# Kernel tuning notes

Hardware: AMD Instinct MI355X
Metric: run time of the kernel (lower is better)

Reference implementation:

```python
import jax, jax.numpy as jnp
import numpy as np

EPS = 1e-5  # torch BatchNorm2d default


def _conv(x, w, padding):
    return jax.lax.conv_general_dilated(
        x, w, window_strides=(1, 1),
        padding=[(padding, padding), (padding, padding)],
        dimension_numbers=("NCHW", "OIHW", "NCHW"))


def _bn(x, gamma, beta):
    # training-mode batchnorm (biased variance), matching nn.BatchNorm2d forward
    mu = x.mean(axis=(0, 2, 3), keepdims=True)
    var = x.var(axis=(0, 2, 3), keepdims=True)
    xn = (x - mu) * jax.lax.rsqrt(var + EPS)
    return gamma[None, :, None, None] * xn + beta[None, :, None, None]


def _ste(x):
    # forward: sign(x); backward: pass gradient where |x| <= 1 (STE)
    m = (jnp.abs(x) <= 1.0).astype(x.dtype)
    s = jax.lax.stop_gradient(jnp.sign(x))
    return s + m * x - jax.lax.stop_gradient(m * x)


def _binconv(x, w, alpha, padding=1):
    # XNOR-style: sign both operands, full-precision conv, scale by alpha
    return _conv(jnp.sign(x), jnp.sign(w), padding) * alpha


def _maxpool2(x):
    return jax.lax.reduce_window(x, -jnp.inf, jax.lax.max,
                                 (1, 1, 2, 2), (1, 1, 2, 2), "VALID")


def setup_inputs() -> dict:
    key = jax.random.key(0)
    ks = jax.random.split(key, 8)

    def kaiming(k, shape):
        fan_out = shape[0] * shape[2] * shape[3]
        std = np.sqrt(2.0 / fan_out)
        return jax.random.normal(k, shape, dtype=jnp.float32) * std

    return {
        "x": jax.random.normal(ks[0], (128, 1, 128, 128), dtype=jnp.float32),
        # first conv (full precision) 1->32, k=3, pad=1
        "w1": kaiming(ks[1], (32, 1, 3, 3)),
        "b1": jnp.zeros((32,), jnp.float32),
        "g1": jnp.ones((32,), jnp.float32),
        "beta1": jnp.zeros((32,), jnp.float32),
        # BinaryConv2d 32->32
        "w2": kaiming(ks[2], (32, 32, 3, 3)),
        "a2": jnp.ones((1,), jnp.float32),
        "g2": jnp.ones((32,), jnp.float32),
        "beta2": jnp.zeros((32,), jnp.float32),
        # BinaryConv2d 32->64
        "w3": kaiming(ks[3], (64, 32, 3, 3)),
        "a3": jnp.ones((1,), jnp.float32),
        "g3": jnp.ones((64,), jnp.float32),
        "beta3": jnp.zeros((64,), jnp.float32),
        # BinaryConv2d 64->128
        "w4": kaiming(ks[4], (128, 64, 3, 3)),
        "a4": jnp.ones((1,), jnp.float32),
        # classifier 128->10
        "wf": jax.random.normal(ks[5], (10, 128), dtype=jnp.float32) * (1.0 / np.sqrt(128.0)),
        "bf": jnp.zeros((10,), jnp.float32),
    }


def reference(x, w1, b1, g1, beta1, w2, a2, g2, beta2, w3, a3, g3, beta3, w4, a4, wf, bf):
    h = _conv(x, w1, padding=1) + b1[None, :, None, None]   # [N,32,128,128]
    h = _bn(h, g1, beta1)
    h = _ste(h)
    h = _binconv(h, w2, a2)                                 # [N,32,128,128]
    h = _maxpool2(h)                                        # [N,32,64,64]
    h = _bn(h, g2, beta2)
    h = _ste(h)
    h = _binconv(h, w3, a3)                                 # [N,64,64,64]
    h = _maxpool2(h)                                        # [N,64,32,32]
    h = _bn(h, g3, beta3)
    h = _ste(h)
    h = _binconv(h, w4, a4)                                 # [N,128,32,32]
    h = h.mean(axis=(2, 3))                                 # AdaptiveAvgPool2d(1) -> [N,128]
    return h @ wf.T + bf                                    # [N,10]
```

## Files before the change

### kernel.cpp

```cpp
#include <hip/hip_runtime.h>
#include <stdint.h>

constexpr int NB = 128;

__global__ void pack_weights_all_kernel(const float* __restrict__ w2, const float* __restrict__ w3,
                                        const float* __restrict__ w4,
                                        uint32_t* __restrict__ wp2, uint32_t* __restrict__ wp3,
                                        uint32_t* __restrict__ wp4)
{
    int idx = blockIdx.x * blockDim.x + threadIdx.x;
    const float* w; uint32_t* o; int ICW, i;
    if (idx < 288)       { w = w2; o = wp2; ICW = 1; i = idx; }
    else if (idx < 864)  { w = w3; o = wp3; ICW = 1; i = idx - 288; }
    else if (idx < 3168) { w = w4; o = wp4; ICW = 2; i = idx - 864; }
    else return;
    int iw = i % ICW;
    int t  = (i / ICW) % 9;
    int oc = i / (9 * ICW);
    int IC = ICW * 32;
    uint32_t word = 0;
    for (int b = 0; b < 32; ++b) {
        float wv = w[(size_t)(oc * IC + (iw * 32 + b)) * 9 + t];
        word |= (wv > 0.f ? 1u : 0u) << b;
    }
    o[i] = word;
}

__global__ void zero_borders_kernel(uint32_t* __restrict__ s1p, uint32_t* __restrict__ s2p,
                                    uint32_t* __restrict__ counters)
{
    int t = blockIdx.x * 256 + threadIdx.x;
    if (t < 4) counters[t] = 0u;
    const int total1 = 128 * 516;
    if (t < total1) {
        int n = t / 516, i = t % 516;
        int r, c;
        if (i < 130)      { r = 0;   c = i; }
        else if (i < 260) { r = 129; c = i - 130; }
        else { int j = i - 260; r = 1 + (j >> 1); c = (j & 1) ? 129 : 0; }
        s1p[(size_t)n * 16900 + r * 130 + c] = 0u;
    }
    int t2 = t - total1;
    const int total2 = 128 * 260;
    if (t2 >= 0 && t2 < total2) {
        int n = t2 / 260, i = t2 % 260;
        int r, c;
        if (i < 66)       { r = 0;  c = i; }
        else if (i < 132) { r = 65; c = i - 66; }
        else { int j = i - 132; r = 1 + (j >> 1); c = (j & 1) ? 65 : 0; }
        s2p[(size_t)n * 4356 + r * 66 + c] = 0u;
    }
}

__device__ __forceinline__ void conv1_load9(const float* __restrict__ x, int p, float* xv)
{
    int n = p >> 14;
    int y = (p >> 7) & 127;
    int c = p & 127;
    const float* xn = x + (size_t)n * 16384;
    #pragma unroll
    for (int ky = 0; ky < 3; ++ky)
    #pragma unroll
    for (int kx = 0; kx < 3; ++kx) {
        int yy = y + ky - 1, cc = c + kx - 1;
        float v = 0.f;
        if (yy >= 0 && yy < 128 && cc >= 0 && cc < 128) v = xn[yy * 128 + cc];
        xv[ky * 3 + kx] = v;
    }
}

__global__ __launch_bounds__(256) void xcorr_kernel(const float* __restrict__ x,
                                                    float* __restrict__ partials)
{
    __shared__ float wbuf[4][64];
    int tid = threadIdx.x;
    float s[9], c[45];
    #pragma unroll
    for (int t = 0; t < 9; ++t) s[t] = 0.f;
    #pragma unroll
    for (int q = 0; q < 45; ++q) c[q] = 0.f;

    int base = blockIdx.x * 256 + tid;
    #pragma unroll 4
    for (int k = 0; k < 16; ++k) {
        float xv[9];
        conv1_load9(x, base + k * 131072, xv);
        #pragma unroll
        for (int t = 0; t < 9; ++t) {
            s[t] += xv[t];
            #pragma unroll
            for (int u = t; u < 9; ++u) {
                int q = t * (19 - t) / 2 + (u - t);
                c[q] = fmaf(xv[t], xv[u], c[q]);
            }
        }
    }
    #pragma unroll
    for (int t = 0; t < 9; ++t) {
        float a = s[t];
        #pragma unroll
        for (int off = 32; off >= 1; off >>= 1) a += __shfl_xor(a, off, 64);
        s[t] = a;
    }
    #pragma unroll
    for (int q = 0; q < 45; ++q) {
        float a = c[q];
        #pragma unroll
        for (int off = 32; off >= 1; off >>= 1) a += __shfl_xor(a, off, 64);
        c[q] = a;
    }
    int lane = tid & 63, wv = tid >> 6;
    if (lane == 0) {
        #pragma unroll
        for (int t = 0; t < 9; ++t) wbuf[wv][t] = s[t];
        #pragma unroll
        for (int q = 0; q < 45; ++q) wbuf[wv][9 + q] = c[q];
    }
    __syncthreads();
    if (tid < 54)
        partials[blockIdx.x * 64 + tid] =
            (wbuf[0][tid] + wbuf[1][tid]) + (wbuf[2][tid] + wbuf[3][tid]);
}

__global__ __launch_bounds__(512) void reduce_ss1_kernel(
    const float* __restrict__ partials, const float* __restrict__ w1, const float* __restrict__ b1,
    const float* __restrict__ g1, const float* __restrict__ be1,
    float* __restrict__ ss, float* __restrict__ w1f)
{
    __shared__ double red[54][8];
    __shared__ double S[9], C[45];
    int tid = threadIdx.x;
    int ch = tid >> 3, part = tid & 7;
    if (ch < 54) {
        double a0 = 0.0, a1 = 0.0, a2 = 0.0, a3 = 0.0;
        #pragma unroll 4
        for (int j = 0; j < 64; ++j) {
            double v = (double)partials[(size_t)(part + 8 * j) * 64 + ch];
            if ((j & 3) == 0) a0 += v;
            else if ((j & 3) == 1) a1 += v;
            else if ((j & 3) == 2) a2 += v;
            else a3 += v;
        }
        red[ch][part] = (a0 + a1) + (a2 + a3);
    }
    __syncthreads();
    if (tid < 54) {
        double a = 0.0;
        #pragma unroll
        for (int i = 0; i < 8; ++i) a += red[tid][i];
        if (tid < 9) S[tid] = a;
        else C[tid - 9] = a;
    }
    __syncthreads();
    if (tid >= 32) return;
    double b = (double)b1[tid];
    double w[9];
    #pragma unroll
    for (int t = 0; t < 9; ++t) w[t] = (double)w1[tid * 9 + t];
    double Sdot = 0.0, Q = 0.0;
    #pragma unroll
    for (int t = 0; t < 9; ++t) {
        Sdot += w[t] * S[t];
        #pragma unroll
        for (int u = t; u < 9; ++u) {
            int q = t * (19 - t) / 2 + (u - t);
            double term = w[t] * w[u] * C[q];
            Q += (u == t) ? term : 2.0 * term;
        }
    }
    const double N = 2097152.0;
    double mu  = Sdot / N + b;
    double ex2 = (Q + 2.0 * b * Sdot) / N + b * b;
    float var = (float)(ex2 - mu * mu);
    float A = g1[tid] * (1.f / sqrtf(var + 1e-5f));
    ss[tid] = A;
    ss[32 + tid] = be1[tid] - (float)mu * A;
    #pragma unroll
    for (int t = 0; t < 9; ++t) w1f[tid * 12 + t] = w1[tid * 9 + t];
    w1f[tid * 12 + 9]  = A;
    w1f[tid * 12 + 10] = fmaf(A, b1[tid], be1[tid] - (float)mu * A);
    w1f[tid * 12 + 11] = 0.f;
}

__global__ __launch_bounds__(256) void conv1_pack4_kernel(
    const float* __restrict__ x, const float* __restrict__ w1f, uint32_t* __restrict__ s1p)
{
    __shared__ float wl[384];
    int tid = threadIdx.x;
    if (tid < 96) ((float4*)wl)[tid] = ((const float4*)w1f)[tid];
    __syncthreads();

    int t = blockIdx.x * 256 + tid;
    int n = t >> 12;
    int y = (t >> 5) & 127;
    int q = t & 31;
    int c0 = q << 2;
    const float* xn = x + (size_t)n * 16384;

    float xv[3][6];
    #pragma unroll
    for (int r = 0; r < 3; ++r) {
        int yy = y - 1 + r;
        bool rv = (yy >= 0) && (yy < 128);
        float4 v = {0.f, 0.f, 0.f, 0.f};
        float lf = 0.f, rt = 0.f;
        if (rv) {
            v = *(const float4*)(xn + yy * 128 + c0);
            if (q != 0)  lf = xn[yy * 128 + c0 - 1];
            if (q != 31) rt = xn[yy * 128 + c0 + 4];
        }
        xv[r][0] = lf; xv[r][1] = v.x; xv[r][2] = v.y;
        xv[r][3] = v.z; xv[r][4] = v.w; xv[r][5] = rt;
    }

    uint32_t word[4] = {0u, 0u, 0u, 0u};
    for (int oc = 0; oc < 32; ++oc) {
        float4 wa = *(const float4*)&wl[oc * 12];
        float4 wb = *(const float4*)&wl[oc * 12 + 4];
        float4 wc = *(const float4*)&wl[oc * 12 + 8];
        float w[9] = {wa.x, wa.y, wa.z, wa.w, wb.x, wb.y, wb.z, wb.w, wc.x};
        #pragma unroll
        for (int i = 0; i < 4; ++i) {
            float a = xv[0][i] * w[0];
            a = fmaf(xv[0][i + 1], w[1], a);
            a = fmaf(xv[0][i + 2], w[2], a);
            a = fmaf(xv[1][i],     w[3], a);
            a = fmaf(xv[1][i + 1], w[4], a);
            a = fmaf(xv[1][i + 2], w[5], a);
            a = fmaf(xv[2][i],     w[6], a);
            a = fmaf(xv[2][i + 1], w[7], a);
            a = fmaf(xv[2][i + 2], w[8], a);
            float vv = fmaf(wc.y, a, wc.z);
            word[i] |= (vv > 0.f ? 1u : 0u) << oc;
        }
    }
    size_t base = (size_t)n * 16900 + (size_t)(y + 1) * 130 + (c0 + 1);
    #pragma unroll
    for (int i = 0; i < 4; ++i) s1p[base + i] = word[i];
}

template<int OC, int PW, int LPW, int MAINB>
__global__ __launch_bounds__(256) void binconv_mainfix_kernel(
    const uint32_t* __restrict__ sp_in, const uint32_t* __restrict__ wp,
    const float* __restrict__ alpha, uint32_t* __restrict__ m16)
{
    constexpr int PS = 2 * PW + 2;
    constexpr int TOTAL = NB * PW * PW;
    __shared__ uint32_t wl[OC * 12];
    int tid = threadIdx.x;
    for (int i = tid; i < OC * 9; i += 256) wl[(i / 9) * 12 + (i % 9)] = wp[i];
    __syncthreads();
    bool useMax = (alpha[0] >= 0.f);

    if ((int)blockIdx.x < MAINB) {
        int p = blockIdx.x * 256 + tid;
        int px = p & (PW - 1), py = (p >> LPW) & (PW - 1), n = p >> (2 * LPW);
        bool border = (px == 0) | (px == PW - 1) | (py == 0) | (py == PW - 1);
        const uint32_t* base = sp_in + (size_t)n * PS * PS + (2 * py) * PS + 2 * px;

        uint32_t xw[16];
        #pragma unroll
        for (int r = 0; r < 4; ++r) {
            uint2 a = *(const uint2*)(base + r * PS);
            uint2 b = *(const uint2*)(base + r * PS + 2);
            xw[r * 4 + 0] = a.x; xw[r * 4 + 1] = a.y;
            xw[r * 4 + 2] = b.x; xw[r * 4 + 3] = b.y;
        }

        uint32_t pend = 0;
        for (int oc = 0; oc < OC; ++oc) {
            uint4 wa = *(const uint4*)&wl[oc * 12];
            uint4 wb = *(const uint4*)&wl[oc * 12 + 4];
            uint32_t w8 = wl[oc * 12 + 8];
            uint32_t w[9] = {wa.x, wa.y, wa.z, wa.w, wb.x, wb.y, wb.z, wb.w, w8};
            int s0 = 0, s1 = 0, s2 = 0, s3 = 0;
            #pragma unroll
            for (int ky = 0; ky < 3; ++ky)
            #pragma unroll
            for (int kx = 0; kx < 3; ++kx) {
                uint32_t wt = w[ky * 3 + kx];
                s0 += __popc(xw[ky * 4 + kx]           ^ wt);
                s1 += __popc(xw[ky * 4 + kx + 1]       ^ wt);
                s2 += __popc(xw[(ky + 1) * 4 + kx]     ^ wt);
                s3 += __popc(xw[(ky + 1) * 4 + kx + 1] ^ wt);
            }
            int sm = useMax ? min(min(s0, s1), min(s2, s3))
                            : max(max(s0, s1), max(s2, s3));
            int m = 288 - 2 * sm;
            if ((oc & 1) == 0) pend = (uint32_t)(uint16_t)(short)m;
            else if (!border)
                m16[(size_t)(oc >> 1) * TOTAL + p] = pend | ((uint32_t)(uint16_t)(short)m << 16);
        }
    } else {
        constexpr int RING = 4 * PW - 4;
        int t = ((int)blockIdx.x - MAINB) * 256 + tid;
        if (t >= NB * RING) return;
        int n = t / RING, r = t % RING;
        int py, px;
        if (r < PW)              { py = 0;      px = r; }
        else if (r < 2 * PW)     { py = PW - 1; px = r - PW; }
        else if (r < 3 * PW - 2) { px = 0;      py = r - 2 * PW + 1; }
        else                     { px = PW - 1; py = r - (3 * PW - 2) + 1; }
        int p = n * PW * PW + py * PW + px;
        const uint32_t* base = sp_in + (size_t)n * PS * PS + (2 * py) * PS + 2 * px;

        uint32_t xw[16], wm[16];
        #pragma unroll
        for (int a = 0; a < 4; ++a) {
            int rr = 2 * py - 1 + a;
            bool rv = (rr >= 0) && (rr < 2 * PW);
            #pragma unroll
            for (int b = 0; b < 4; ++b) {
                int cc = 2 * px - 1 + b;
                bool v = rv && (cc >= 0) && (cc < 2 * PW);
                wm[a * 4 + b] = v ? 0xFFFFFFFFu : 0u;
                xw[a * 4 + b] = base[a * PS + b];
            }
        }
        int cnt[4];
        #pragma unroll
        for (int a2 = 0; a2 < 2; ++a2)
        #pragma unroll
        for (int b2 = 0; b2 < 2; ++b2) {
            int cc = 0;
            #pragma unroll
            for (int ky = 0; ky < 3; ++ky)
            #pragma unroll
            for (int kx = 0; kx < 3; ++kx)
                cc += (int)(wm[(a2 + ky) * 4 + (b2 + kx)] & 1u);
            cnt[a2 * 2 + b2] = cc * 32;
        }

        uint32_t pend = 0;
        for (int oc = 0; oc < OC; ++oc) {
            uint4 wa = *(const uint4*)&wl[oc * 12];
            uint4 wb = *(const uint4*)&wl[oc * 12 + 4];
            uint32_t w8 = wl[oc * 12 + 8];
            uint32_t w[9] = {wa.x, wa.y, wa.z, wa.w, wb.x, wb.y, wb.z, wb.w, w8};
            int v[4];
            #pragma unroll
            for (int a2 = 0; a2 < 2; ++a2)
            #pragma unroll
            for (int b2 = 0; b2 < 2; ++b2) {
                int pop = 0;
                #pragma unroll
                for (int ky = 0; ky < 3; ++ky)
                #pragma unroll
                for (int kx = 0; kx < 3; ++kx) {
                    int idx = (a2 + ky) * 4 + (b2 + kx);
                    pop += __popc((xw[idx] ^ w[ky * 3 + kx]) & wm[idx]);
                }
                v[a2 * 2 + b2] = cnt[a2 * 2 + b2] - 2 * pop;
            }
            int m = useMax ? max(max(v[0], v[1]), max(v[2], v[3]))
                           : min(min(v[0], v[1]), min(v[2], v[3]));
            if ((oc & 1) == 0) pend = (uint32_t)(uint16_t)(short)m;
            else m16[(size_t)(oc >> 1) * TOTAL + p] = pend | ((uint32_t)(uint16_t)(short)m << 16);
        }
    }
}

template<int PIXELS, int CHUNKS, int OC>
__global__ __launch_bounds__(256) void stats16_fin_kernel(
    const uint32_t* __restrict__ m16, double* __restrict__ pd, uint32_t* __restrict__ counter,
    const float* __restrict__ gamma, const float* __restrict__ beta,
    const float* __restrict__ alpha, float inv_n, float* __restrict__ ss)
{
    __shared__ int wb[4][4];
    int bid = blockIdx.x;
    int q = bid / CHUNKS, ch = bid % CHUNKS;
    const uint32_t* pl = m16 + (size_t)q * PIXELS + (size_t)ch * (PIXELS / CHUNKS);
    int tid = threadIdx.x;
    int s0 = 0, s1 = 0, q0 = 0, q1 = 0;
    #pragma unroll 4
    for (int j = 0; j < PIXELS / CHUNKS / 256; ++j) {
        uint32_t u = pl[tid + j * 256];
        int m0 = (int)(short)(u & 0xffffu);
        int m1 = (int)u >> 16;
        s0 += m0; s1 += m1;
        q0 += m0 * m0; q1 += m1 * m1;
    }
    #pragma unroll
    for (int off = 32; off >= 1; off >>= 1) {
        s0 += __shfl_xor(s0, off, 64); s1 += __shfl_xor(s1, off, 64);
        q0 += __shfl_xor(q0, off, 64); q1 += __shfl_xor(q1, off, 64);
    }
    int lane = tid & 63, w = tid >> 6;
    if (lane == 0) { wb[w][0] = s0; wb[w][1] = s1; wb[w][2] = q0; wb[w][3] = q1; }
    __syncthreads();
    if (tid < 4)
        pd[(size_t)bid * 4 + tid] =
            (double)((long long)wb[0][tid] + wb[1][tid] + wb[2][tid] + wb[3][tid]);

    __threadfence();
    __shared__ int lastflag;
    if (tid == 0) lastflag = (atomicAdd(counter, 1u) == (uint32_t)(gridDim.x - 1)) ? 1 : 0;
    __syncthreads();
    if (!lastflag) return;
    __threadfence();
    if (tid == 0) *counter = 0u;

    __shared__ double sums[2 * OC];
    if (tid < 2 * OC) {
        bool issq = tid >= OC;
        int c = issq ? tid - OC : tid;
        int qq = c >> 1;
        int slot = (issq ? 2 : 0) + (c & 1);
        double a = 0.0;
        #pragma unroll 4
        for (int i = 0; i < CHUNKS; ++i)
            a += pd[(size_t)(qq * CHUNKS + i) * 4 + slot];
        sums[tid] = a;
    }
    __syncthreads();
    if (tid < OC) {
        double al = (double)alpha[0];
        float mu  = (float)(sums[tid] * al * (double)inv_n);
        float ex2 = (float)(sums[OC + tid] * al * al * (double)inv_n);
        float var = ex2 - mu * mu;
        float A = gamma[tid] * (1.f / sqrtf(var + 1e-5f));
        ss[tid] = A;
        ss[OC + tid] = beta[tid] - mu * A;
    }
}

template<int OC, int PW, int LPW, bool PADOUT>
__global__ __launch_bounds__(256) void binconv_pack_kernel(
    const uint32_t* __restrict__ m16, const float* __restrict__ alpha,
    const float* __restrict__ ss, void* __restrict__ sout)
{
    constexpr int TOTAL = NB * PW * PW;
    __shared__ float Ap[OC], Bp[OC];
    int tid = threadIdx.x;
    if (tid < OC) { Ap[tid] = ss[tid] * alpha[0]; Bp[tid] = ss[OC + tid]; }
    __syncthreads();
    int p = blockIdx.x * 256 + tid;
    uint64_t word = 0;
    #pragma unroll
    for (int q = 0; q < OC / 2; ++q) {
        uint32_t u = m16[(size_t)q * TOTAL + p];
        int m0 = (int)(short)(u & 0xffffu);
        int m1 = (int)u >> 16;
        float v0 = fmaf(Ap[2 * q],     (float)m0, Bp[2 * q]);
        float v1 = fmaf(Ap[2 * q + 1], (float)m1, Bp[2 * q + 1]);
        word |= (v0 > 0.f ? 1ull : 0ull) << (2 * q);
        word |= (v1 > 0.f ? 1ull : 0ull) << (2 * q + 1);
    }
    if constexpr (PADOUT) {
        int px = p & (PW - 1), py = (p >> LPW) & (PW - 1), n = p >> (2 * LPW);
        ((uint32_t*)sout)[(size_t)n * (PW + 2) * (PW + 2) + (py + 1) * (PW + 2) + (px + 1)]
            = (uint32_t)word;
    } else {
        ((uint64_t*)sout)[p] = word;
    }
}

__global__ __launch_bounds__(256) void conv4_partial_kernel(
    const uint64_t* __restrict__ s3, const uint64_t* __restrict__ wp4,
    float* __restrict__ p4)
{
    __shared__ uint64_t xt[192];
    __shared__ uint64_t wl[1152];
    __shared__ float red[256];
    int b = blockIdx.x;
    int n = b >> 3, s = b & 7;
    int tid = threadIdx.x;
    for (int i = tid; i < 192; i += 256) {
        int row = 4 * s - 1 + (i >> 5);
        int col = i & 31;
        xt[i] = (row >= 0 && row < 32) ? s3[(size_t)n * 1024 + row * 32 + col] : 0ull;
    }
    for (int i = tid; i < 1152; i += 256) wl[i] = wp4[i];
    __syncthreads();
    int oc = tid & 127, h = tid >> 7;
    uint64_t wr[9];
    #pragma unroll
    for (int t = 0; t < 9; ++t) wr[t] = wl[oc * 9 + t];
    int acc = 0;
    #pragma unroll
    for (int ry = 0; ry < 2; ++ry) {
        int lry = 2 * h + ry;
        int y = 4 * s + lry;
        for (int x = 0; x < 32; ++x) {
            int pop = 0, c = 0;
            #pragma unroll
            for (int ky = 0; ky < 3; ++ky) {
                int yy = y + ky - 1;
                if (yy < 0 || yy >= 32) continue;
                int lrow = lry + ky;
                #pragma unroll
                for (int kx = 0; kx < 3; ++kx) {
                    int xx = x + kx - 1;
                    if (xx < 0 || xx >= 32) continue;
                    pop += __popcll(xt[lrow * 32 + xx] ^ wr[ky * 3 + kx]);
                    c += 64;
                }
            }
            acc += c - 2 * pop;
        }
    }
    red[tid] = (float)acc;
    __syncthreads();
    if (tid < 128)
        p4[(size_t)b * 128 + tid] = red[tid] + red[tid + 128];
}

__global__ __launch_bounds__(128) void mean_linear_kernel(
    const float* __restrict__ p4, const float* __restrict__ alpha4,
    const float* __restrict__ wf, const float* __restrict__ bf, float* __restrict__ out)
{
    __shared__ float ml[128];
    int n = blockIdx.x, tid = threadIdx.x;
    float a = 0.f;
    #pragma unroll
    for (int s = 0; s < 8; ++s)
        a += p4[(size_t)((n * 8 + s) * 128) + tid];
    ml[tid] = a * alpha4[0] * (1.f / 1024.f);
    __syncthreads();
    if (tid < 10) {
        const float* w = wf + tid * 128;
        float acc = bf[tid];
        #pragma unroll 4
        for (int i = 0; i < 128; ++i) acc = fmaf(ml[i], w[i], acc);
        out[n * 10 + tid] = acc;
    }
}

extern "C" void kernel_launch(void* const* d_in, const int* in_sizes, int n_in,
                              void* d_out, int out_size, void* d_ws, size_t ws_size,
                              hipStream_t stream)
{
    const float* x   = (const float*)d_in[0];
    const float* w1  = (const float*)d_in[1];
    const float* b1  = (const float*)d_in[2];
    const float* g1  = (const float*)d_in[3];
    const float* be1 = (const float*)d_in[4];
    const float* w2  = (const float*)d_in[5];
    const float* a2  = (const float*)d_in[6];
    const float* g2  = (const float*)d_in[7];
    const float* be2 = (const float*)d_in[8];
    const float* w3  = (const float*)d_in[9];
    const float* a3  = (const float*)d_in[10];
    const float* g3  = (const float*)d_in[11];
    const float* be3 = (const float*)d_in[12];
    const float* w4  = (const float*)d_in[13];
    const float* a4  = (const float*)d_in[14];
    const float* wf  = (const float*)d_in[15];
    const float* bf  = (const float*)d_in[16];
    float* out = (float*)d_out;

    uint8_t* ws = (uint8_t*)d_ws;
    size_t off = 0;
    auto alloc = [&](size_t bytes) -> void* {
        void* p = ws + off;
        off += (bytes + 255) & ~(size_t)255;
        return p;
    };
    uint32_t* wp2 = (uint32_t*)alloc(288 * 4);
    uint32_t* wp3 = (uint32_t*)alloc(576 * 4);
    uint32_t* wp4 = (uint32_t*)alloc(2304 * 4);
    float* ss1 = (float*)alloc(64 * 4);
    float* ss2 = (float*)alloc(64 * 4);
    float* ss3 = (float*)alloc(128 * 4);
    float* w1f = (float*)alloc(384 * 4);
    uint32_t* counters = (uint32_t*)alloc(4 * 4);
    double* pd    = (double*)alloc(2048 * 8);
    float* partials = (float*)alloc((size_t)512 * 64 * 4);
    uint32_t* s1p = (uint32_t*)alloc((size_t)128 * 16900 * 4);
    uint32_t* s2p = (uint32_t*)alloc((size_t)128 * 4356 * 4);
    uint64_t* s3  = (uint64_t*)alloc((size_t)128 * 1024 * 8);
    float* p4    = (float*)alloc((size_t)1024 * 128 * 4);
    uint32_t* m16_2 = (uint32_t*)alloc((size_t)16 * 524288 * 4);
    uint32_t* m16_3 = (uint32_t*)alloc((size_t)32 * 131072 * 4);

    zero_borders_kernel<<<388, 256, 0, stream>>>(s1p, s2p, counters);

    pack_weights_all_kernel<<<13, 256, 0, stream>>>(w2, w3, w4, wp2, wp3, wp4);

    xcorr_kernel<<<512, 256, 0, stream>>>(x, partials);
    reduce_ss1_kernel<<<1, 512, 0, stream>>>(partials, w1, b1, g1, be1, ss1, w1f);
    conv1_pack4_kernel<<<2048, 256, 0, stream>>>(x, w1f, s1p);

    binconv_mainfix_kernel<32, 64, 6, 2048><<<2048 + 126, 256, 0, stream>>>(s1p, wp2, a2, m16_2);
    stats16_fin_kernel<524288, 32, 32><<<512, 256, 0, stream>>>(m16_2, pd, counters + 0,
                                                                g2, be2, a2, 1.f / 524288.f, ss2);
    binconv_pack_kernel<32, 64, 6, true><<<2048, 256, 0, stream>>>(m16_2, a2, ss2, (void*)s2p);

    binconv_mainfix_kernel<64, 32, 5, 512><<<512 + 62, 256, 0, stream>>>(s2p, wp3, a3, m16_3);
    stats16_fin_kernel<131072, 8, 64><<<256, 256, 0, stream>>>(m16_3, pd, counters + 1,
                                                               g3, be3, a3, 1.f / 131072.f, ss3);
    binconv_pack_kernel<64, 32, 5, false><<<512, 256, 0, stream>>>(m16_3, a3, ss3, (void*)s3);

    conv4_partial_kernel<<<1024, 256, 0, stream>>>(s3, (const uint64_t*)wp4, p4);
    mean_linear_kernel<<<128, 128, 0, stream>>>(p4, a4, wf, bf, out);
}
```

Measured before the change: 265.4 us.

## Fuse prologue kernels, fold mean-linear into conv4, split binconv main/fix launches

```diff
diff --git a/kernel.cpp b/kernel.cpp
--- a/kernel.cpp
+++ b/kernel.cpp
@@ -2,55 +2,6 @@
 #include <stdint.h>
 
 constexpr int NB = 128;
-
-__global__ void pack_weights_all_kernel(const float* __restrict__ w2, const float* __restrict__ w3,
-                                        const float* __restrict__ w4,
-                                        uint32_t* __restrict__ wp2, uint32_t* __restrict__ wp3,
-                                        uint32_t* __restrict__ wp4)
-{
-    int idx = blockIdx.x * blockDim.x + threadIdx.x;
-    const float* w; uint32_t* o; int ICW, i;
-    if (idx < 288)       { w = w2; o = wp2; ICW = 1; i = idx; }
-    else if (idx < 864)  { w = w3; o = wp3; ICW = 1; i = idx - 288; }
-    else if (idx < 3168) { w = w4; o = wp4; ICW = 2; i = idx - 864; }
-    else return;
-    int iw = i % ICW;
-    int t  = (i / ICW) % 9;
-    int oc = i / (9 * ICW);
-    int IC = ICW * 32;
-    uint32_t word = 0;
-    for (int b = 0; b < 32; ++b) {
-        float wv = w[(size_t)(oc * IC + (iw * 32 + b)) * 9 + t];
-        word |= (wv > 0.f ? 1u : 0u) << b;
-    }
-    o[i] = word;
-}
-
-__global__ void zero_borders_kernel(uint32_t* __restrict__ s1p, uint32_t* __restrict__ s2p,
-                                    uint32_t* __restrict__ counters)
-{
-    int t = blockIdx.x * 256 + threadIdx.x;
-    if (t < 4) counters[t] = 0u;
-    const int total1 = 128 * 516;
-    if (t < total1) {
-        int n = t / 516, i = t % 516;
-        int r, c;
-        if (i < 130)      { r = 0;   c = i; }
-        else if (i < 260) { r = 129; c = i - 130; }
-        else { int j = i - 260; r = 1 + (j >> 1); c = (j & 1) ? 129 : 0; }
-        s1p[(size_t)n * 16900 + r * 130 + c] = 0u;
-    }
-    int t2 = t - total1;
-    const int total2 = 128 * 260;
-    if (t2 >= 0 && t2 < total2) {
-        int n = t2 / 260, i = t2 % 260;
-        int r, c;
-        if (i < 66)       { r = 0;  c = i; }
-        else if (i < 132) { r = 65; c = i - 66; }
-        else { int j = i - 132; r = 1 + (j >> 1); c = (j & 1) ? 65 : 0; }
-        s2p[(size_t)n * 4356 + r * 66 + c] = 0u;
-    }
-}
 
 __device__ __forceinline__ void conv1_load9(const float* __restrict__ x, int p, float* xv)
 {
@@ -69,18 +20,69 @@
     }
 }
 
-__global__ __launch_bounds__(256) void xcorr_kernel(const float* __restrict__ x,
-                                                    float* __restrict__ partials)
+__global__ __launch_bounds__(256) void prologue_kernel(
+    uint32_t* __restrict__ s1p, uint32_t* __restrict__ s2p, uint32_t* __restrict__ counters,
+    const float* __restrict__ w2, const float* __restrict__ w3, const float* __restrict__ w4,
+    uint32_t* __restrict__ wp2, uint32_t* __restrict__ wp3, uint32_t* __restrict__ wp4,
+    const float* __restrict__ x, float* __restrict__ partials)
 {
     __shared__ float wbuf[4][64];
-    int tid = threadIdx.x;
+    int bid = blockIdx.x;
+    int tid = threadIdx.x;
+
+    if (bid < 388) {
+        int t = bid * 256 + tid;
+        if (t < 132) counters[t] = 0u;
+        const int total1 = 128 * 516;
+        if (t < total1) {
+            int n = t / 516, i = t % 516;
+            int r, c;
+            if (i < 130)      { r = 0;   c = i; }
+            else if (i < 260) { r = 129; c = i - 130; }
+            else { int j = i - 260; r = 1 + (j >> 1); c = (j & 1) ? 129 : 0; }
+            s1p[(size_t)n * 16900 + r * 130 + c] = 0u;
+        }
+        int t2 = t - total1;
+        const int total2 = 128 * 260;
+        if (t2 >= 0 && t2 < total2) {
+            int n = t2 / 260, i = t2 % 260;
+            int r, c;
+            if (i < 66)       { r = 0;  c = i; }
+            else if (i < 132) { r = 65; c = i - 66; }
+            else { int j = i - 132; r = 1 + (j >> 1); c = (j & 1) ? 65 : 0; }
+            s2p[(size_t)n * 4356 + r * 66 + c] = 0u;
+        }
+        return;
+    }
+
+    if (bid < 401) {
+        int idx = (bid - 388) * 256 + tid;
+        const float* w; uint32_t* o; int ICW, i;
+        if (idx < 288)       { w = w2; o = wp2; ICW = 1; i = idx; }
+        else if (idx < 864)  { w = w3; o = wp3; ICW = 1; i = idx - 288; }
+        else if (idx < 3168) { w = w4; o = wp4; ICW = 2; i = idx - 864; }
+        else return;
+        int iw = i % ICW;
+        int t  = (i / ICW) % 9;
+        int oc = i / (9 * ICW);
+        int IC = ICW * 32;
+        uint32_t word = 0;
+        for (int b = 0; b < 32; ++b) {
+            float wv = w[(size_t)(oc * IC + (iw * 32 + b)) * 9 + t];
+            word |= (wv > 0.f ? 1u : 0u) << b;
+        }
+        o[i] = word;
+        return;
+    }
+
+    int xb = bid - 401;
     float s[9], c[45];
     #pragma unroll
     for (int t = 0; t < 9; ++t) s[t] = 0.f;
     #pragma unroll
     for (int q = 0; q < 45; ++q) c[q] = 0.f;
 
-    int base = blockIdx.x * 256 + tid;
+    int base = xb * 256 + tid;
     #pragma unroll 4
     for (int k = 0; k < 16; ++k) {
         float xv[9];
@@ -118,7 +120,7 @@
     }
     __syncthreads();
     if (tid < 54)
-        partials[blockIdx.x * 64 + tid] =
+        partials[xb * 64 + tid] =
             (wbuf[0][tid] + wbuf[1][tid]) + (wbuf[2][tid] + wbuf[3][tid]);
 }
 
@@ -182,65 +184,35 @@
     w1f[tid * 12 + 11] = 0.f;
 }
 
-__global__ __launch_bounds__(256) void conv1_pack4_kernel(
+__global__ __launch_bounds__(256) void conv1_pack3_kernel(
     const float* __restrict__ x, const float* __restrict__ w1f, uint32_t* __restrict__ s1p)
 {
-    __shared__ float wl[384];
-    int tid = threadIdx.x;
-    if (tid < 96) ((float4*)wl)[tid] = ((const float4*)w1f)[tid];
-    __syncthreads();
-
-    int t = blockIdx.x * 256 + tid;
-    int n = t >> 12;
-    int y = (t >> 5) & 127;
-    int q = t & 31;
-    int c0 = q << 2;
-    const float* xn = x + (size_t)n * 16384;
-
-    float xv[3][6];
-    #pragma unroll
-    for (int r = 0; r < 3; ++r) {
-        int yy = y - 1 + r;
-        bool rv = (yy >= 0) && (yy < 128);
-        float4 v = {0.f, 0.f, 0.f, 0.f};
-        float lf = 0.f, rt = 0.f;
-        if (rv) {
-            v = *(const float4*)(xn + yy * 128 + c0);
-            if (q != 0)  lf = xn[yy * 128 + c0 - 1];
-            if (q != 31) rt = xn[yy * 128 + c0 + 4];
-        }
-        xv[r][0] = lf; xv[r][1] = v.x; xv[r][2] = v.y;
-        xv[r][3] = v.z; xv[r][4] = v.w; xv[r][5] = rt;
-    }
-
-    uint32_t word[4] = {0u, 0u, 0u, 0u};
+    int p = blockIdx.x * 256 + threadIdx.x;
+    float xv[9];
+    conv1_load9(x, p, xv);
+    int n = p >> 14, y = (p >> 7) & 127, c = p & 127;
+
+    uint32_t word = 0;
+    #pragma unroll 4
     for (int oc = 0; oc < 32; ++oc) {
-        float4 wa = *(const float4*)&wl[oc * 12];
-        float4 wb = *(const float4*)&wl[oc * 12 + 4];
-        float4 wc = *(const float4*)&wl[oc * 12 + 8];
-        float w[9] = {wa.x, wa.y, wa.z, wa.w, wb.x, wb.y, wb.z, wb.w, wc.x};
-        #pragma unroll
-        for (int i = 0; i < 4; ++i) {
-            float a = xv[0][i] * w[0];
-            a = fmaf(xv[0][i + 1], w[1], a);
-            a = fmaf(xv[0][i + 2], w[2], a);
-            a = fmaf(xv[1][i],     w[3], a);
-            a = fmaf(xv[1][i + 1], w[4], a);
-            a = fmaf(xv[1][i + 2], w[5], a);
-            a = fmaf(xv[2][i],     w[6], a);
-            a = fmaf(xv[2][i + 1], w[7], a);
-            a = fmaf(xv[2][i + 2], w[8], a);
-            float vv = fmaf(wc.y, a, wc.z);
-            word[i] |= (vv > 0.f ? 1u : 0u) << oc;
-        }
-    }
-    size_t base = (size_t)n * 16900 + (size_t)(y + 1) * 130 + (c0 + 1);
-    #pragma unroll
-    for (int i = 0; i < 4; ++i) s1p[base + i] = word[i];
-}
-
-template<int OC, int PW, int LPW, int MAINB>
-__global__ __launch_bounds__(256) void binconv_mainfix_kernel(
+        const float* wf = w1f + oc * 12;
+        float a = xv[0] * wf[0];
+        a = fmaf(xv[1], wf[1], a);
+        a = fmaf(xv[2], wf[2], a);
+        a = fmaf(xv[3], wf[3], a);
+        a = fmaf(xv[4], wf[4], a);
+        a = fmaf(xv[5], wf[5], a);
+        a = fmaf(xv[6], wf[6], a);
+        a = fmaf(xv[7], wf[7], a);
+        a = fmaf(xv[8], wf[8], a);
+        float v = fmaf(wf[9], a, wf[10]);
+        word |= (v > 0.f ? 1u : 0u) << oc;
+    }
+    s1p[(size_t)n * 16900 + (y + 1) * 130 + (c + 1)] = word;
+}
+
+template<int OC, int PW, int LPW>
+__global__ __launch_bounds__(256) void binconv_main_kernel(
     const uint32_t* __restrict__ sp_in, const uint32_t* __restrict__ wp,
     const float* __restrict__ alpha, uint32_t* __restrict__ m16)
 {
@@ -251,112 +223,120 @@
     for (int i = tid; i < OC * 9; i += 256) wl[(i / 9) * 12 + (i % 9)] = wp[i];
     __syncthreads();
     bool useMax = (alpha[0] >= 0.f);
-
-    if ((int)blockIdx.x < MAINB) {
-        int p = blockIdx.x * 256 + tid;
-        int px = p & (PW - 1), py = (p >> LPW) & (PW - 1), n = p >> (2 * LPW);
-        bool border = (px == 0) | (px == PW - 1) | (py == 0) | (py == PW - 1);
-        const uint32_t* base = sp_in + (size_t)n * PS * PS + (2 * py) * PS + 2 * px;
-
-        uint32_t xw[16];
-        #pragma unroll
-        for (int r = 0; r < 4; ++r) {
-            uint2 a = *(const uint2*)(base + r * PS);
-            uint2 b = *(const uint2*)(base + r * PS + 2);
-            xw[r * 4 + 0] = a.x; xw[r * 4 + 1] = a.y;
-            xw[r * 4 + 2] = b.x; xw[r * 4 + 3] = b.y;
-        }
-
-        uint32_t pend = 0;
-        for (int oc = 0; oc < OC; ++oc) {
-            uint4 wa = *(const uint4*)&wl[oc * 12];
-            uint4 wb = *(const uint4*)&wl[oc * 12 + 4];
-            uint32_t w8 = wl[oc * 12 + 8];
-            uint32_t w[9] = {wa.x, wa.y, wa.z, wa.w, wb.x, wb.y, wb.z, wb.w, w8};
-            int s0 = 0, s1 = 0, s2 = 0, s3 = 0;
+    int p = blockIdx.x * 256 + tid;
+    int px = p & (PW - 1), py = (p >> LPW) & (PW - 1), n = p >> (2 * LPW);
+    const uint32_t* base = sp_in + (size_t)n * PS * PS + (2 * py) * PS + 2 * px;
+
+    uint32_t xw[16];
+    #pragma unroll
+    for (int r = 0; r < 4; ++r) {
+        uint2 a = *(const uint2*)(base + r * PS);
+        uint2 b = *(const uint2*)(base + r * PS + 2);
+        xw[r * 4 + 0] = a.x; xw[r * 4 + 1] = a.y;
+        xw[r * 4 + 2] = b.x; xw[r * 4 + 3] = b.y;
+    }
+
+    uint32_t pend = 0;
+    for (int oc = 0; oc < OC; ++oc) {
+        uint4 wa = *(const uint4*)&wl[oc * 12];
+        uint4 wb = *(const uint4*)&wl[oc * 12 + 4];
+        uint32_t w8 = wl[oc * 12 + 8];
+        uint32_t w[9] = {wa.x, wa.y, wa.z, wa.w, wb.x, wb.y, wb.z, wb.w, w8};
+        int s0 = 0, s1 = 0, s2 = 0, s3 = 0;
+        #pragma unroll
+        for (int ky = 0; ky < 3; ++ky)
+        #pragma unroll
+        for (int kx = 0; kx < 3; ++kx) {
+            uint32_t wt = w[ky * 3 + kx];
+            s0 += __popc(xw[ky * 4 + kx]           ^ wt);
+            s1 += __popc(xw[ky * 4 + kx + 1]       ^ wt);
+            s2 += __popc(xw[(ky + 1) * 4 + kx]     ^ wt);
+            s3 += __popc(xw[(ky + 1) * 4 + kx + 1] ^ wt);
+        }
+        int sm = useMax ? min(min(s0, s1), min(s2, s3))
+                        : max(max(s0, s1), max(s2, s3));
+        int m = 288 - 2 * sm;
+        if ((oc & 1) == 0) pend = (uint32_t)(uint16_t)(short)m;
+        else m16[(size_t)(oc >> 1) * TOTAL + p] = pend | ((uint32_t)(uint16_t)(short)m << 16);
+    }
+}
+
+template<int OC, int PW>
+__global__ __launch_bounds__(256) void binconv_fix_kernel(
+    const uint32_t* __restrict__ sp_in, const uint32_t* __restrict__ wp,
+    const float* __restrict__ alpha, uint32_t* __restrict__ m16)
+{
+    constexpr int PS = 2 * PW + 2;
+    constexpr int TOTAL = NB * PW * PW;
+    constexpr int RING = 4 * PW - 4;
+    __shared__ uint32_t wl[OC * 12];
+    int tid = threadIdx.x;
+    for (int i = tid; i < OC * 9; i += 256) wl[(i / 9) * 12 + (i % 9)] = wp[i];
+    __syncthreads();
+    bool useMax = (alpha[0] >= 0.f);
+    int t = blockIdx.x * 256 + tid;
+    if (t >= NB * RING) return;
+    int n = t / RING, r = t % RING;
+    int py, px;
+    if (r < PW)              { py = 0;      px = r; }
+    else if (r < 2 * PW)     { py = PW - 1; px = r - PW; }
+    else if (r < 3 * PW - 2) { px = 0;      py = r - 2 * PW + 1; }
+    else                     { px = PW - 1; py = r - (3 * PW - 2) + 1; }
+    int p = n * PW * PW + py * PW + px;
+    const uint32_t* base = sp_in + (size_t)n * PS * PS + (2 * py) * PS + 2 * px;
+
+    uint32_t xw[16], wm[16];
+    #pragma unroll
+    for (int a = 0; a < 4; ++a) {
+        int rr = 2 * py - 1 + a;
+        bool rv = (rr >= 0) && (rr < 2 * PW);
+        #pragma unroll
+        for (int b = 0; b < 4; ++b) {
+            int cc = 2 * px - 1 + b;
+            bool v = rv && (cc >= 0) && (cc < 2 * PW);
+            wm[a * 4 + b] = v ? 0xFFFFFFFFu : 0u;
+            xw[a * 4 + b] = base[a * PS + b];
+        }
+    }
+    int cnt[4];
+    #pragma unroll
+    for (int a2 = 0; a2 < 2; ++a2)
+    #pragma unroll
+    for (int b2 = 0; b2 < 2; ++b2) {
+        int cc = 0;
+        #pragma unroll
+        for (int ky = 0; ky < 3; ++ky)
+        #pragma unroll
+        for (int kx = 0; kx < 3; ++kx)
+            cc += (int)(wm[(a2 + ky) * 4 + (b2 + kx)] & 1u);
+        cnt[a2 * 2 + b2] = cc * 32;
+    }
+
+    uint32_t pend = 0;
+    for (int oc = 0; oc < OC; ++oc) {
+        uint4 wa = *(const uint4*)&wl[oc * 12];
+        uint4 wb = *(const uint4*)&wl[oc * 12 + 4];
+        uint32_t w8 = wl[oc * 12 + 8];
+        uint32_t w[9] = {wa.x, wa.y, wa.z, wa.w, wb.x, wb.y, wb.z, wb.w, w8};
+        int v[4];
+        #pragma unroll
+        for (int a2 = 0; a2 < 2; ++a2)
+        #pragma unroll
+        for (int b2 = 0; b2 < 2; ++b2) {
+            int pop = 0;
             #pragma unroll
             for (int ky = 0; ky < 3; ++ky)
             #pragma unroll
             for (int kx = 0; kx < 3; ++kx) {
-                uint32_t wt = w[ky * 3 + kx];
-                s0 += __popc(xw[ky * 4 + kx]           ^ wt);
-                s1 += __popc(xw[ky * 4 + kx + 1]       ^ wt);
-                s2 += __popc(xw[(ky + 1) * 4 + kx]     ^ wt);
-                s3 += __popc(xw[(ky + 1) * 4 + kx + 1] ^ wt);
+                int idx = (a2 + ky) * 4 + (b2 + kx);
+                pop += __popc((xw[idx] ^ w[ky * 3 + kx]) & wm[idx]);
             }
-            int sm = useMax ? min(min(s0, s1), min(s2, s3))
-                            : max(max(s0, s1), max(s2, s3));
-            int m = 288 - 2 * sm;
-            if ((oc & 1) == 0) pend = (uint32_t)(uint16_t)(short)m;
-            else if (!border)
-                m16[(size_t)(oc >> 1) * TOTAL + p] = pend | ((uint32_t)(uint16_t)(short)m << 16);
-        }
-    } else {
-        constexpr int RING = 4 * PW - 4;
-        int t = ((int)blockIdx.x - MAINB) * 256 + tid;
-        if (t >= NB * RING) return;
-        int n = t / RING, r = t % RING;
-        int py, px;
-        if (r < PW)              { py = 0;      px = r; }
-        else if (r < 2 * PW)     { py = PW - 1; px = r - PW; }
-        else if (r < 3 * PW - 2) { px = 0;      py = r - 2 * PW + 1; }
-        else                     { px = PW - 1; py = r - (3 * PW - 2) + 1; }
-        int p = n * PW * PW + py * PW + px;
-        const uint32_t* base = sp_in + (size_t)n * PS * PS + (2 * py) * PS + 2 * px;
-
-        uint32_t xw[16], wm[16];
-        #pragma unroll
-        for (int a = 0; a < 4; ++a) {
-            int rr = 2 * py - 1 + a;
-            bool rv = (rr >= 0) && (rr < 2 * PW);
-            #pragma unroll
-            for (int b = 0; b < 4; ++b) {
-                int cc = 2 * px - 1 + b;
-                bool v = rv && (cc >= 0) && (cc < 2 * PW);
-                wm[a * 4 + b] = v ? 0xFFFFFFFFu : 0u;
-                xw[a * 4 + b] = base[a * PS + b];
-            }
-        }
-        int cnt[4];
-        #pragma unroll
-        for (int a2 = 0; a2 < 2; ++a2)
-        #pragma unroll
-        for (int b2 = 0; b2 < 2; ++b2) {
-            int cc = 0;
-            #pragma unroll
-            for (int ky = 0; ky < 3; ++ky)
-            #pragma unroll
-            for (int kx = 0; kx < 3; ++kx)
-                cc += (int)(wm[(a2 + ky) * 4 + (b2 + kx)] & 1u);
-            cnt[a2 * 2 + b2] = cc * 32;
-        }
-
-        uint32_t pend = 0;
-        for (int oc = 0; oc < OC; ++oc) {
-            uint4 wa = *(const uint4*)&wl[oc * 12];
-            uint4 wb = *(const uint4*)&wl[oc * 12 + 4];
-            uint32_t w8 = wl[oc * 12 + 8];
-            uint32_t w[9] = {wa.x, wa.y, wa.z, wa.w, wb.x, wb.y, wb.z, wb.w, w8};
-            int v[4];
-            #pragma unroll
-            for (int a2 = 0; a2 < 2; ++a2)
-            #pragma unroll
-            for (int b2 = 0; b2 < 2; ++b2) {
-                int pop = 0;
-                #pragma unroll
-                for (int ky = 0; ky < 3; ++ky)
-                #pragma unroll
-                for (int kx = 0; kx < 3; ++kx) {
-                    int idx = (a2 + ky) * 4 + (b2 + kx);
-                    pop += __popc((xw[idx] ^ w[ky * 3 + kx]) & wm[idx]);
-                }
-                v[a2 * 2 + b2] = cnt[a2 * 2 + b2] - 2 * pop;
-            }
-            int m = useMax ? max(max(v[0], v[1]), max(v[2], v[3]))
-                           : min(min(v[0], v[1]), min(v[2], v[3]));
-            if ((oc & 1) == 0) pend = (uint32_t)(uint16_t)(short)m;
-            else m16[(size_t)(oc >> 1) * TOTAL + p] = pend | ((uint32_t)(uint16_t)(short)m << 16);
-        }
+            v[a2 * 2 + b2] = cnt[a2 * 2 + b2] - 2 * pop;
+        }
+        int m = useMax ? max(max(v[0], v[1]), max(v[2], v[3]))
+                       : min(min(v[0], v[1]), min(v[2], v[3]));
+        if ((oc & 1) == 0) pend = (uint32_t)(uint16_t)(short)m;
+        else m16[(size_t)(oc >> 1) * TOTAL + p] = pend | ((uint32_t)(uint16_t)(short)m << 16);
     }
 }
 
@@ -398,7 +378,6 @@
     __syncthreads();
     if (!lastflag) return;
     __threadfence();
-    if (tid == 0) *counter = 0u;
 
     __shared__ double sums[2 * OC];
     if (tid < 2 * OC) {
@@ -455,13 +434,17 @@
     }
 }
 
-__global__ __launch_bounds__(256) void conv4_partial_kernel(
+__global__ __launch_bounds__(256) void conv4_ml_kernel(
     const uint64_t* __restrict__ s3, const uint64_t* __restrict__ wp4,
-    float* __restrict__ p4)
+    const float* __restrict__ alpha4, const float* __restrict__ wf,
+    const float* __restrict__ bf, uint32_t* __restrict__ imgcnt,
+    float* __restrict__ p4, float* __restrict__ out)
 {
     __shared__ uint64_t xt[192];
     __shared__ uint64_t wl[1152];
     __shared__ float red[256];
+    __shared__ float ml[128];
+    __shared__ int last;
     int b = blockIdx.x;
     int n = b >> 3, s = b & 7;
     int tid = threadIdx.x;
@@ -503,26 +486,27 @@
     __syncthreads();
     if (tid < 128)
         p4[(size_t)b * 128 + tid] = red[tid] + red[tid + 128];
-}
-
-__global__ __launch_bounds__(128) void mean_linear_kernel(
-    const float* __restrict__ p4, const float* __restrict__ alpha4,
-    const float* __restrict__ wf, const float* __restrict__ bf, float* __restrict__ out)
-{
-    __shared__ float ml[128];
-    int n = blockIdx.x, tid = threadIdx.x;
-    float a = 0.f;
-    #pragma unroll
-    for (int s = 0; s < 8; ++s)
-        a += p4[(size_t)((n * 8 + s) * 128) + tid];
-    ml[tid] = a * alpha4[0] * (1.f / 1024.f);
+
+    __threadfence();
+    if (tid == 0) last = (atomicAdd(&imgcnt[n], 1u) == 7u) ? 1 : 0;
+    __syncthreads();
+    if (!last) return;
+    __threadfence();
+
+    if (tid < 128) {
+        float a = 0.f;
+        #pragma unroll
+        for (int ss4 = 0; ss4 < 8; ++ss4)
+            a += p4[(size_t)((n * 8 + ss4) * 128) + tid];
+        ml[tid] = a * alpha4[0] * (1.f / 1024.f);
+    }
     __syncthreads();
     if (tid < 10) {
         const float* w = wf + tid * 128;
-        float acc = bf[tid];
+        float a2 = bf[tid];
         #pragma unroll 4
-        for (int i = 0; i < 128; ++i) acc = fmaf(ml[i], w[i], acc);
-        out[n * 10 + tid] = acc;
+        for (int i = 0; i < 128; ++i) a2 = fmaf(ml[i], w[i], a2);
+        out[n * 10 + tid] = a2;
     }
 }
 
@@ -563,7 +547,7 @@
     float* ss2 = (float*)alloc(64 * 4);
     float* ss3 = (float*)alloc(128 * 4);
     float* w1f = (float*)alloc(384 * 4);
-    uint32_t* counters = (uint32_t*)alloc(4 * 4);
+    uint32_t* counters = (uint32_t*)alloc(132 * 4);
     double* pd    = (double*)alloc(2048 * 8);
     float* partials = (float*)alloc((size_t)512 * 64 * 4);
     uint32_t* s1p = (uint32_t*)alloc((size_t)128 * 16900 * 4);
@@ -573,24 +557,23 @@
     uint32_t* m16_2 = (uint32_t*)alloc((size_t)16 * 524288 * 4);
     uint32_t* m16_3 = (uint32_t*)alloc((size_t)32 * 131072 * 4);
 
-    zero_borders_kernel<<<388, 256, 0, stream>>>(s1p, s2p, counters);
-
-    pack_weights_all_kernel<<<13, 256, 0, stream>>>(w2, w3, w4, wp2, wp3, wp4);
-
-    xcorr_kernel<<<512, 256, 0, stream>>>(x, partials);
+    prologue_kernel<<<913, 256, 0, stream>>>(s1p, s2p, counters,
+                                             w2, w3, w4, wp2, wp3, wp4, x, partials);
     reduce_ss1_kernel<<<1, 512, 0, stream>>>(partials, w1, b1, g1, be1, ss1, w1f);
-    conv1_pack4_kernel<<<2048, 256, 0, stream>>>(x, w1f, s1p);
-
-    binconv_mainfix_kernel<32, 64, 6, 2048><<<2048 + 126, 256, 0, stream>>>(s1p, wp2, a2, m16_2);
+    conv1_pack3_kernel<<<8192, 256, 0, stream>>>(x, w1f, s1p);
+
+    binconv_main_kernel<32, 64, 6><<<2048, 256, 0, stream>>>(s1p, wp2, a2, m16_2);
+    binconv_fix_kernel<32, 64><<<126, 256, 0, stream>>>(s1p, wp2, a2, m16_2);
     stats16_fin_kernel<524288, 32, 32><<<512, 256, 0, stream>>>(m16_2, pd, counters + 0,
                                                                 g2, be2, a2, 1.f / 524288.f, ss2);
     binconv_pack_kernel<32, 64, 6, true><<<2048, 256, 0, stream>>>(m16_2, a2, ss2, (void*)s2p);
 
-    binconv_mainfix_kernel<64, 32, 5, 512><<<512 + 62, 256, 0, stream>>>(s2p, wp3, a3, m16_3);
+    binconv_main_kernel<64, 32, 5><<<512, 256, 0, stream>>>(s2p, wp3, a3, m16_3);
+    binconv_fix_kernel<64, 32><<<62, 256, 0, stream>>>(s2p, wp3, a3, m16_3);
     stats16_fin_kernel<131072, 8, 64><<<256, 256, 0, stream>>>(m16_3, pd, counters + 1,
                                                                g3, be3, a3, 1.f / 131072.f, ss3);
     binconv_pack_kernel<64, 32, 5, false><<<512, 256, 0, stream>>>(m16_3, a3, ss3, (void*)s3);
 
-    conv4_partial_kernel<<<1024, 256, 0, stream>>>(s3, (const uint64_t*)wp4, p4);
-    mean_linear_kernel<<<128, 128, 0, stream>>>(p4, a4, wf, bf, out);
-}
+    conv4_ml_kernel<<<1024, 256, 0, stream>>>(s3, (const uint64_t*)wp4, a4, wf, bf,
+                                              counters + 2, p4, out);
+}
```

Result: slower. 357.1 us (median of 3 runs) (+34.6%).
